# Kernel optimization log

Hardware: AMD Instinct MI355X
Metric: run time of the kernel (lower is better)

## Reference

```python
import jax, jax.numpy as jnp
import numpy as np

N = 100000   # nodes
E = 1600000  # edges
D = 128      # in_channels
H = 64       # hidden_channels
G = 64       # graphs in batch
C = 2        # num_classes


def _linear_init(key, fin, fout):
    s = 1.0 / np.sqrt(fin)
    kw, kb = jax.random.split(key)
    w = jax.random.uniform(kw, (fin, fout), jnp.float32, -s, s)
    b = jax.random.uniform(kb, (fout,), jnp.float32, -s, s)
    return w, b


def setup_inputs() -> dict:
    key = jax.random.key(0)
    ks = jax.random.split(key, 12)
    x = jax.random.normal(ks[0], (N, D), jnp.float32)
    edge_index = jax.random.randint(ks[1], (2, E), 0, N)
    batch = jnp.sort(jax.random.randint(ks[2], (N,), 0, G))
    inp = {"x": x, "edge_index": edge_index, "batch": batch}
    fins = [D, H, H]
    for i, fin in enumerate(fins):
        w1, b1 = _linear_init(ks[3 + 2 * i], fin, H)
        w2, b2 = _linear_init(ks[4 + 2 * i], H, H)
        inp[f"l{i}_w1"], inp[f"l{i}_b1"] = w1, b1
        inp[f"l{i}_w2"], inp[f"l{i}_b2"] = w2, b2
    inp["lin1_w"], inp["lin1_b"] = _linear_init(ks[9], H, H)
    inp["lin2_w"], inp["lin2_b"] = _linear_init(ks[10], H, C)
    return inp


def _gin_conv(h, edge_index, w1, b1, w2, b2):
    # sum-aggregate neighbor features: dst += h[src]  (eps = 0)
    agg = jax.ops.segment_sum(h[edge_index[0]], edge_index[1], num_segments=N)
    z = h + agg
    return jnp.maximum(z @ w1 + b1, 0.0) @ w2 + b2


def reference(x, edge_index, batch,
              l0_w1, l0_b1, l0_w2, l0_b2,
              l1_w1, l1_b1, l1_w2, l1_b2,
              l2_w1, l2_b1, l2_w2, l2_b2,
              lin1_w, lin1_b, lin2_w, lin2_b):
    params = [(l0_w1, l0_b1, l0_w2, l0_b2),
              (l1_w1, l1_b1, l1_w2, l1_b2),
              (l2_w1, l2_b1, l2_w2, l2_b2)]
    h = x
    for (w1, b1, w2, b2) in params:
        h = jnp.maximum(_gin_conv(h, edge_index, w1, b1, w2, b2), 0.0)
        # dropout is identity in eval mode
    # global mean pool over graph ids
    sums = jax.ops.segment_sum(h, batch, num_segments=G)          # [G, H]
    cnt = jax.ops.segment_sum(jnp.ones((N,), jnp.float32), batch, num_segments=G)
    pooled = sums / jnp.maximum(cnt, 1.0)[:, None]
    out = jnp.maximum(pooled @ lin1_w + lin1_b, 0.0)
    return out @ lin2_w + lin2_b  # [G, C]
```

## Files before the change

kernel.cpp:

```cpp
#include <hip/hip_runtime.h>
#include <hip/hip_bf16.h>


__device__ inline unsigned short f2bf(float f) {
    union { __hip_bfloat16 b; unsigned short u; } cv;
    cv.b = __float2bfloat16(f);
    return cv.u;
}
__device__ inline float bflo(unsigned int v) {
    union { unsigned int u; float f; } c; c.u = v << 16; return c.f;
}
__device__ inline float bfhi(unsigned int v) {
    union { unsigned int u; float f; } c; c.u = v & 0xffff0000u; return c.f;
}

__global__ __launch_bounds__(1024) void zero1024_kernel(int* __restrict__ p) {
    p[threadIdx.x] = 0;
}

__global__ __launch_bounds__(256) void count_buckets_kernel(
    const int* __restrict__ ei, int* __restrict__ gcount, int E_) {
    __shared__ int hist[1024];
    const int tid = threadIdx.x;
    for (int i = tid; i < 1024; i += 256) hist[i] = 0;
    __syncthreads();
    const int base = blockIdx.x * 2048;
#pragma unroll
    for (int i = 0; i < 8; i++) {
        int e = base + i * 256 + tid;
        if (e < E_) atomicAdd(&hist[ei[E_ + e] >> 9], 1);
    }
    __syncthreads();
    for (int i = tid; i < 1024; i += 256)
        if (hist[i]) atomicAdd(&gcount[i], hist[i]);
}

__global__ __launch_bounds__(1024) void scan_buckets_kernel(
    const int* __restrict__ gcount, int* __restrict__ bbase,
    int* __restrict__ gcursor, int* __restrict__ rowptr, int K, int E_, int n) {
    __shared__ int sd[1024];
    const int tid = threadIdx.x;
    int v = (tid < K) ? gcount[tid] : 0;
    sd[tid] = v;
    __syncthreads();
    for (int off = 1; off < 1024; off <<= 1) {
        int x = (tid >= off) ? sd[tid - off] : 0;
        __syncthreads();
        sd[tid] += x;
        __syncthreads();
    }
    if (tid < K) {
        int excl = sd[tid] - v;
        bbase[tid] = excl;
        gcursor[tid] = excl;
    }
    if (tid == 0) {
        bbase[K] = E_;
        rowptr[n] = E_;
    }
}

__global__ __launch_bounds__(256) void bucketize_kernel(
    const int* __restrict__ ei, int* __restrict__ gcursor,
    unsigned* __restrict__ bpack, int E_) {
    __shared__ int hist[1024];
    __shared__ int gbase[1024];
    const int tid = threadIdx.x;
    for (int i = tid; i < 1024; i += 256) hist[i] = 0;
    __syncthreads();
    const int base = blockIdx.x * 2048;
    int bkt[8], rnk[8];
    unsigned pk[8];
#pragma unroll
    for (int i = 0; i < 8; i++) {
        int e = base + i * 256 + tid;
        bkt[i] = -1;
        if (e < E_) {
            int s = ei[e];
            int d = ei[E_ + e];
            bkt[i] = d >> 9;
            pk[i] = (unsigned)s | ((unsigned)(d & 511) << 22);
            rnk[i] = atomicAdd(&hist[bkt[i]], 1);
        }
    }
    __syncthreads();
    for (int i = tid; i < 1024; i += 256)
        if (hist[i]) gbase[i] = atomicAdd(&gcursor[i], hist[i]);
    __syncthreads();
#pragma unroll
    for (int i = 0; i < 8; i++)
        if (bkt[i] >= 0) bpack[gbase[bkt[i]] + rnk[i]] = pk[i];
}

__global__ __launch_bounds__(256) void build_csr_kernel(
    const unsigned* __restrict__ bpack, const int* __restrict__ bbase,
    int* __restrict__ rowptr, int* __restrict__ col, int n) {
    __shared__ int cnt[512];
    __shared__ int sp[256];
    const int tid = threadIdx.x;
    const int b = blockIdx.x;
    const int nstart = b << 9;
    const int estart = bbase[b];
    const int eend = bbase[b + 1];
    cnt[tid] = 0;
    cnt[tid + 256] = 0;
    __syncthreads();
    for (int e = estart + tid; e < eend; e += 256)
        atomicAdd(&cnt[bpack[e] >> 22], 1);
    __syncthreads();
    const int v0 = cnt[tid * 2], v1 = cnt[tid * 2 + 1];
    const int s = v0 + v1;
    sp[tid] = s;
    __syncthreads();
    for (int off = 1; off < 256; off <<= 1) {
        int x = (tid >= off) ? sp[tid - off] : 0;
        __syncthreads();
        sp[tid] += x;
        __syncthreads();
    }
    const int excl = sp[tid] - s;
    cnt[tid * 2] = excl;
    cnt[tid * 2 + 1] = excl + v0;
    const int node0 = nstart + tid * 2;
    if (node0 < n) rowptr[node0] = estart + excl;
    if (node0 + 1 < n) rowptr[node0 + 1] = estart + excl + v0;
    __syncthreads();
    for (int e = estart + tid; e < eend; e += 256) {
        unsigned p = bpack[e];
        int pos = estart + atomicAdd(&cnt[p >> 22], 1);
        col[pos] = (int)(p & 0x3FFFFFu);
    }
}

__global__ __launch_bounds__(256) void proj128_kernel(
    const float* __restrict__ x, unsigned short* __restrict__ y,
    const float* __restrict__ w, int n) {
    constexpr int STR = 66;
    __shared__ unsigned int xs[64 * STR];
    const int tid = threadIdx.x;
    const int tile = blockIdx.x;
    for (int idx = tid; idx < 64 * 64; idx += 256) {
        int r = idx >> 6;
        int c = idx & 63;
        int node = tile * 64 + r;
        float2 v = make_float2(0.f, 0.f);
        if (node < n) v = *reinterpret_cast<const float2*>(x + (size_t)node * 128 + c * 2);
        xs[r * STR + c] = (unsigned)f2bf(v.x) | ((unsigned)f2bf(v.y) << 16);
    }
    __syncthreads();
    const int lane = tid & 63;
    const int j0 = __builtin_amdgcn_readfirstlane(tid >> 6) << 4;
    float a[16];
#pragma unroll
    for (int jj = 0; jj < 16; jj++) a[jj] = 0.f;
    for (int k = 0; k < 128; k += 8) {
        unsigned p0 = xs[lane * STR + k / 2 + 0];
        unsigned p1 = xs[lane * STR + k / 2 + 1];
        unsigned p2 = xs[lane * STR + k / 2 + 2];
        unsigned p3 = xs[lane * STR + k / 2 + 3];
        const float tv[8] = {bflo(p0), bfhi(p0), bflo(p1), bfhi(p1),
                             bflo(p2), bfhi(p2), bflo(p3), bfhi(p3)};
#pragma unroll
        for (int kk = 0; kk < 8; kk++)
#pragma unroll
            for (int jj = 0; jj < 16; jj++)
                a[jj] = fmaf(tv[kk], w[(k + kk) * 64 + j0 + jj], a[jj]);
    }
    const int node = tile * 64 + lane;
    if (node < n) {
        unsigned pk[8];
#pragma unroll
        for (int jj = 0; jj < 8; jj++)
            pk[jj] = (unsigned)f2bf(a[2 * jj]) | ((unsigned)f2bf(a[2 * jj + 1]) << 16);
        uint4* orow = reinterpret_cast<uint4*>(y + (size_t)node * 64 + j0);
        orow[0] = make_uint4(pk[0], pk[1], pk[2], pk[3]);
        orow[1] = make_uint4(pk[4], pk[5], pk[6], pk[7]);
    }
}

template <bool LAST>
__global__ __launch_bounds__(256) void fused_layer_kernel(
    const unsigned short* __restrict__ yin,
    const int* __restrict__ rowptr, const int* __restrict__ col,
    const float* __restrict__ b1,
    const float* __restrict__ w2, const float* __restrict__ b2,
    const float* __restrict__ w1n,
    unsigned short* __restrict__ yout, float* __restrict__ hout, int n) {
    constexpr int STR = 66;
    __shared__ float tl[64 * STR];
    const int tid = threadIdx.x;
    const int tile = blockIdx.x;
    const int lane = tid & 63;
    const int wv = __builtin_amdgcn_readfirstlane(tid >> 6);
    const int q = lane >> 4;
    const int fl = lane & 15;
    const uint2* y64 = reinterpret_cast<const uint2*>(yin);
    const float4 b1v = *reinterpret_cast<const float4*>(b1 + 4 * fl);

    for (int i = 0; i < 16; ++i) {
        const int node = tile * 64 + wv * 16 + i;
        if (node >= n) break;
        const int rs = rowptr[node];
        const int deg = rowptr[node + 1] - rs;
        float ax, ay, az, aw;
        {
            const uint2 sv = y64[(size_t)node * 16 + fl];
            const float m = (q == 0) ? 1.f : 0.f;
            ax = m * bflo(sv.x); ay = m * bfhi(sv.x);
            az = m * bflo(sv.y); aw = m * bfhi(sv.y);
        }
        int p = q;
        for (; p + 12 < deg; p += 16) {
            const int c0 = col[rs + p];
            const int c1 = col[rs + p + 4];
            const int c2 = col[rs + p + 8];
            const int c3 = col[rs + p + 12];
            const uint2 v0 = y64[(size_t)c0 * 16 + fl];
            const uint2 v1 = y64[(size_t)c1 * 16 + fl];
            const uint2 v2 = y64[(size_t)c2 * 16 + fl];
            const uint2 v3 = y64[(size_t)c3 * 16 + fl];
            ax += bflo(v0.x); ay += bfhi(v0.x); az += bflo(v0.y); aw += bfhi(v0.y);
            ax += bflo(v1.x); ay += bfhi(v1.x); az += bflo(v1.y); aw += bfhi(v1.y);
            ax += bflo(v2.x); ay += bfhi(v2.x); az += bflo(v2.y); aw += bfhi(v2.y);
            ax += bflo(v3.x); ay += bfhi(v3.x); az += bflo(v3.y); aw += bfhi(v3.y);
        }
        for (; p + 4 < deg; p += 8) {
            const int c0 = col[rs + p];
            const int c1 = col[rs + p + 4];
            const uint2 v0 = y64[(size_t)c0 * 16 + fl];
            const uint2 v1 = y64[(size_t)c1 * 16 + fl];
            ax += bflo(v0.x); ay += bfhi(v0.x); az += bflo(v0.y); aw += bfhi(v0.y);
            ax += bflo(v1.x); ay += bfhi(v1.x); az += bflo(v1.y); aw += bfhi(v1.y);
        }
        for (; p < deg; p += 4) {
            const int c = col[rs + p];
            const uint2 v = y64[(size_t)c * 16 + fl];
            ax += bflo(v.x); ay += bfhi(v.x); az += bflo(v.y); aw += bfhi(v.y);
        }
        ax += __shfl_xor(ax, 16); ay += __shfl_xor(ay, 16);
        az += __shfl_xor(az, 16); aw += __shfl_xor(aw, 16);
        ax += __shfl_xor(ax, 32); ay += __shfl_xor(ay, 32);
        az += __shfl_xor(az, 32); aw += __shfl_xor(aw, 32);
        if (q == 0) {
            const int row = wv * 16 + i;
            *reinterpret_cast<float2*>(&tl[row * STR + 4 * fl]) =
                make_float2(fmaxf(ax + b1v.x, 0.f), fmaxf(ay + b1v.y, 0.f));
            *reinterpret_cast<float2*>(&tl[row * STR + 4 * fl + 2]) =
                make_float2(fmaxf(az + b1v.z, 0.f), fmaxf(aw + b1v.w, 0.f));
        }
    }
    __syncthreads();

    const int j0 = wv << 4;
    const int node = tile * 64 + lane;
    float a[16];
#pragma unroll
    for (int jj = 0; jj < 16; jj++) a[jj] = b2[j0 + jj];
    for (int k = 0; k < 64; k += 8) {
        float2 t0 = *reinterpret_cast<const float2*>(&tl[lane * STR + k]);
        float2 t1 = *reinterpret_cast<const float2*>(&tl[lane * STR + k + 2]);
        float2 t2 = *reinterpret_cast<const float2*>(&tl[lane * STR + k + 4]);
        float2 t3 = *reinterpret_cast<const float2*>(&tl[lane * STR + k + 6]);
        const float tv[8] = {t0.x, t0.y, t1.x, t1.y, t2.x, t2.y, t3.x, t3.y};
#pragma unroll
        for (int kk = 0; kk < 8; kk++)
#pragma unroll
            for (int jj = 0; jj < 16; jj++)
                a[jj] = fmaf(tv[kk], w2[(k + kk) * 64 + j0 + jj], a[jj]);
    }
#pragma unroll
    for (int jj = 0; jj < 16; jj++) a[jj] = fmaxf(a[jj], 0.f);

    if (LAST) {
        if (node < n) {
            float* orow = hout + (size_t)node * 64 + j0;
#pragma unroll
            for (int jj = 0; jj < 16; jj += 4) {
                *reinterpret_cast<float4*>(orow + jj) =
                    make_float4(a[jj], a[jj + 1], a[jj + 2], a[jj + 3]);
            }
        }
    } else {
        __syncthreads();
#pragma unroll
        for (int jj = 0; jj < 16; jj++) tl[lane * STR + j0 + jj] = a[jj];
        __syncthreads();
        float a2[16];
#pragma unroll
        for (int jj = 0; jj < 16; jj++) a2[jj] = 0.f;
        for (int k = 0; k < 64; k += 8) {
            float2 t0 = *reinterpret_cast<const float2*>(&tl[lane * STR + k]);
            float2 t1 = *reinterpret_cast<const float2*>(&tl[lane * STR + k + 2]);
            float2 t2 = *reinterpret_cast<const float2*>(&tl[lane * STR + k + 4]);
            float2 t3 = *reinterpret_cast<const float2*>(&tl[lane * STR + k + 6]);
            const float tv[8] = {t0.x, t0.y, t1.x, t1.y, t2.x, t2.y, t3.x, t3.y};
#pragma unroll
            for (int kk = 0; kk < 8; kk++)
#pragma unroll
                for (int jj = 0; jj < 16; jj++)
                    a2[jj] = fmaf(tv[kk], w1n[(k + kk) * 64 + j0 + jj], a2[jj]);
        }
        if (node < n) {
            unsigned pk[8];
#pragma unroll
            for (int jj = 0; jj < 8; jj++)
                pk[jj] = (unsigned)f2bf(a2[2 * jj]) | ((unsigned)f2bf(a2[2 * jj + 1]) << 16);
            uint4* orow = reinterpret_cast<uint4*>(yout + (size_t)node * 64 + j0);
            orow[0] = make_uint4(pk[0], pk[1], pk[2], pk[3]);
            orow[1] = make_uint4(pk[4], pk[5], pk[6], pk[7]);
        }
    }
}

#define POOL_PARTS 16
__global__ __launch_bounds__(256) void pool_partial_kernel(
    const float* __restrict__ h, const int* __restrict__ batch,
    float* __restrict__ partials, int n) {
    const int g = blockIdx.x >> 4;
    const int part = blockIdx.x & 15;
    const int tid = threadIdx.x;
    auto lb = [&](int key) {
        int lo = 0, hi = n;
        while (lo < hi) {
            int mid = (lo + hi) >> 1;
            if (batch[mid] < key) lo = mid + 1;
            else hi = mid;
        }
        return lo;
    };
    const int lo = lb(g), hi = lb(g + 1);
    const int cnt = hi - lo;
    const int s0 = lo + (int)(((long long)cnt * part) / POOL_PARTS);
    const int s1 = lo + (int)(((long long)cnt * (part + 1)) / POOL_PARTS);

    const int f = tid & 63;
    const int qq = tid >> 6;
    float s = 0.f;
    for (int i = s0 + qq; i < s1; i += 4) s += h[(size_t)i * 64 + f];

    __shared__ float red[256];
    red[tid] = s;
    __syncthreads();
    if (tid < 64) {
        partials[(size_t)blockIdx.x * 64 + tid] =
            red[tid] + red[tid + 64] + red[tid + 128] + red[tid + 192];
    }
}

__global__ __launch_bounds__(64) void pool_head_kernel(
    const float* __restrict__ partials, const int* __restrict__ batch,
    const float* __restrict__ l1w, const float* __restrict__ l1b,
    const float* __restrict__ l2w, const float* __restrict__ l2b,
    float* __restrict__ out, int n) {
    const int g = blockIdx.x;
    const int tid = threadIdx.x;
    auto lb = [&](int key) {
        int lo = 0, hi = n;
        while (lo < hi) {
            int mid = (lo + hi) >> 1;
            if (batch[mid] < key) lo = mid + 1;
            else hi = mid;
        }
        return lo;
    };
    const int cnt = lb(g + 1) - lb(g);

    __shared__ float pooled[64];
    __shared__ float r[64];
    float v = 0.f;
#pragma unroll
    for (int p = 0; p < POOL_PARTS; p++)
        v += partials[(size_t)(g * POOL_PARTS + p) * 64 + tid];
    pooled[tid] = v / (float)((cnt > 1) ? cnt : 1);
    __syncthreads();
    float a = l1b[tid];
    for (int k = 0; k < 64; k++) a = fmaf(pooled[k], l1w[k * 64 + tid], a);
    r[tid] = fmaxf(a, 0.f);
    __syncthreads();
    if (tid < 2) {
        float a2 = l2b[tid];
        for (int k = 0; k < 64; k++) a2 = fmaf(r[k], l2w[k * 2 + tid], a2);
        out[g * 2 + tid] = a2;
    }
}


extern "C" void kernel_launch(void* const* d_in, const int* in_sizes, int n_in,
                              void* d_out, int out_size, void* d_ws, size_t ws_size,
                              hipStream_t stream) {
    const float* x    = (const float*)d_in[0];
    const int* ei     = (const int*)d_in[1];
    const int* batch  = (const int*)d_in[2];
    const float* l0w1 = (const float*)d_in[3];
    const float* l0b1 = (const float*)d_in[4];
    const float* l0w2 = (const float*)d_in[5];
    const float* l0b2 = (const float*)d_in[6];
    const float* l1w1 = (const float*)d_in[7];
    const float* l1b1 = (const float*)d_in[8];
    const float* l1w2 = (const float*)d_in[9];
    const float* l1b2 = (const float*)d_in[10];
    const float* l2w1 = (const float*)d_in[11];
    const float* l2b1 = (const float*)d_in[12];
    const float* l2w2 = (const float*)d_in[13];
    const float* l2b2 = (const float*)d_in[14];
    const float* lin1w = (const float*)d_in[15];
    const float* lin1b = (const float*)d_in[16];
    const float* lin2w = (const float*)d_in[17];
    const float* lin2b = (const float*)d_in[18];
    float* out = (float*)d_out;

    const int N  = in_sizes[2];
    const int E_ = in_sizes[1] / 2;
    const int K  = (N + 511) >> 9;
    const int G  = out_size / 2;

    char* ws = (char*)d_ws;
    size_t off = 0;
    auto alloc = [&](size_t bytes) {
        void* p = ws + off;
        off += (bytes + 255) & ~(size_t)255;
        return p;
    };
    int* rowptr  = (int*)alloc((size_t)(N + 1) * 4);
    int* col     = (int*)alloc((size_t)E_ * 4);
    int* gcount  = (int*)alloc(1024 * 4);
    int* bbase   = (int*)alloc(1025 * 4);
    int* gcursor = (int*)alloc(1024 * 4);
    float* partials = (float*)alloc((size_t)G * POOL_PARTS * 64 * 4);
    unsigned short* yA = (unsigned short*)alloc((size_t)N * 64 * 2);
    unsigned short* yB = (unsigned short*)alloc((size_t)N * 64 * 2);
    float* hbuf  = (float*)alloc((size_t)N * 64 * 4);
    unsigned* bpack = (unsigned*)hbuf;
    (void)ws_size;

    const int nch = (E_ + 2047) / 2048;

    zero1024_kernel<<<1, 1024, 0, stream>>>(gcount);
    count_buckets_kernel<<<nch, 256, 0, stream>>>(ei, gcount, E_);
    scan_buckets_kernel<<<1, 1024, 0, stream>>>(gcount, bbase, gcursor, rowptr, K, E_, N);
    bucketize_kernel<<<nch, 256, 0, stream>>>(ei, gcursor, bpack, E_);
    build_csr_kernel<<<K, 256, 0, stream>>>(bpack, bbase, rowptr, col, N);

    const int ntiles = (N + 63) / 64;

    proj128_kernel<<<ntiles, 256, 0, stream>>>(x, yA, l0w1, N);
    fused_layer_kernel<false><<<ntiles, 256, 0, stream>>>(
        yA, rowptr, col, l0b1, l0w2, l0b2, l1w1, yB, nullptr, N);
    fused_layer_kernel<false><<<ntiles, 256, 0, stream>>>(
        yB, rowptr, col, l1b1, l1w2, l1b2, l2w1, yA, nullptr, N);
    fused_layer_kernel<true><<<ntiles, 256, 0, stream>>>(
        yA, rowptr, col, l2b1, l2w2, l2b2, nullptr, nullptr, hbuf, N);

    pool_partial_kernel<<<G * POOL_PARTS, 256, 0, stream>>>(hbuf, batch, partials, N);
    pool_head_kernel<<<G, 64, 0, stream>>>(partials, batch, lin1w, lin1b, lin2w, lin2b, out, N);
}
```

Before: 316.4 us.

## Store projected features in chunked planes and gather per 16-feature chunk

The bf16 projected features are written as four planes of 16 features per node instead of one 64-feature row. The aggregation loop then gathers one plane at a time, with 8 lanes per edge and 8 edges per wave step, shrinking the random-access working set per pass to improve cache hit rates. The trade-off is re-reading rowptr/col four times, narrower 32-byte gathers, and extra shuffle reductions.

```diff
diff --git a/kernel.cpp b/kernel.cpp
--- a/kernel.cpp
+++ b/kernel.cpp
@@ -149,7 +149,8 @@
     }
     __syncthreads();
     const int lane = tid & 63;
-    const int j0 = __builtin_amdgcn_readfirstlane(tid >> 6) << 4;
+    const int wv = __builtin_amdgcn_readfirstlane(tid >> 6);
+    const int j0 = wv << 4;
     float a[16];
 #pragma unroll
     for (int jj = 0; jj < 16; jj++) a[jj] = 0.f;
@@ -172,9 +173,10 @@
 #pragma unroll
         for (int jj = 0; jj < 8; jj++)
             pk[jj] = (unsigned)f2bf(a[2 * jj]) | ((unsigned)f2bf(a[2 * jj + 1]) << 16);
-        uint4* orow = reinterpret_cast<uint4*>(y + (size_t)node * 64 + j0);
-        orow[0] = make_uint4(pk[0], pk[1], pk[2], pk[3]);
-        orow[1] = make_uint4(pk[4], pk[5], pk[6], pk[7]);
+        unsigned* yo = reinterpret_cast<unsigned*>(y) + (size_t)wv * n * 8 + (size_t)node * 8;
+        uint4* o = reinterpret_cast<uint4*>(yo);
+        o[0] = make_uint4(pk[0], pk[1], pk[2], pk[3]);
+        o[1] = make_uint4(pk[4], pk[5], pk[6], pk[7]);
     }
 }
 
@@ -192,61 +194,48 @@
     const int tile = blockIdx.x;
     const int lane = tid & 63;
     const int wv = __builtin_amdgcn_readfirstlane(tid >> 6);
-    const int q = lane >> 4;
-    const int fl = lane & 15;
-    const uint2* y64 = reinterpret_cast<const uint2*>(yin);
-    const float4 b1v = *reinterpret_cast<const float4*>(b1 + 4 * fl);
-
-    for (int i = 0; i < 16; ++i) {
-        const int node = tile * 64 + wv * 16 + i;
-        if (node >= n) break;
-        const int rs = rowptr[node];
-        const int deg = rowptr[node + 1] - rs;
-        float ax, ay, az, aw;
-        {
-            const uint2 sv = y64[(size_t)node * 16 + fl];
-            const float m = (q == 0) ? 1.f : 0.f;
-            ax = m * bflo(sv.x); ay = m * bfhi(sv.x);
-            az = m * bflo(sv.y); aw = m * bfhi(sv.y);
-        }
-        int p = q;
-        for (; p + 12 < deg; p += 16) {
-            const int c0 = col[rs + p];
-            const int c1 = col[rs + p + 4];
-            const int c2 = col[rs + p + 8];
-            const int c3 = col[rs + p + 12];
-            const uint2 v0 = y64[(size_t)c0 * 16 + fl];
-            const uint2 v1 = y64[(size_t)c1 * 16 + fl];
-            const uint2 v2 = y64[(size_t)c2 * 16 + fl];
-            const uint2 v3 = y64[(size_t)c3 * 16 + fl];
-            ax += bflo(v0.x); ay += bfhi(v0.x); az += bflo(v0.y); aw += bfhi(v0.y);
-            ax += bflo(v1.x); ay += bfhi(v1.x); az += bflo(v1.y); aw += bfhi(v1.y);
-            ax += bflo(v2.x); ay += bfhi(v2.x); az += bflo(v2.y); aw += bfhi(v2.y);
-            ax += bflo(v3.x); ay += bfhi(v3.x); az += bflo(v3.y); aw += bfhi(v3.y);
-        }
-        for (; p + 4 < deg; p += 8) {
-            const int c0 = col[rs + p];
-            const int c1 = col[rs + p + 4];
-            const uint2 v0 = y64[(size_t)c0 * 16 + fl];
-            const uint2 v1 = y64[(size_t)c1 * 16 + fl];
-            ax += bflo(v0.x); ay += bfhi(v0.x); az += bflo(v0.y); aw += bfhi(v0.y);
-            ax += bflo(v1.x); ay += bfhi(v1.x); az += bflo(v1.y); aw += bfhi(v1.y);
-        }
-        for (; p < deg; p += 4) {
-            const int c = col[rs + p];
-            const uint2 v = y64[(size_t)c * 16 + fl];
-            ax += bflo(v.x); ay += bfhi(v.x); az += bflo(v.y); aw += bfhi(v.y);
-        }
-        ax += __shfl_xor(ax, 16); ay += __shfl_xor(ay, 16);
-        az += __shfl_xor(az, 16); aw += __shfl_xor(aw, 16);
-        ax += __shfl_xor(ax, 32); ay += __shfl_xor(ay, 32);
-        az += __shfl_xor(az, 32); aw += __shfl_xor(aw, 32);
-        if (q == 0) {
-            const int row = wv * 16 + i;
-            *reinterpret_cast<float2*>(&tl[row * STR + 4 * fl]) =
-                make_float2(fmaxf(ax + b1v.x, 0.f), fmaxf(ay + b1v.y, 0.f));
-            *reinterpret_cast<float2*>(&tl[row * STR + 4 * fl + 2]) =
-                make_float2(fmaxf(az + b1v.z, 0.f), fmaxf(aw + b1v.w, 0.f));
+    const int e8 = lane >> 3;
+    const int f8 = lane & 7;
+    const unsigned int* y32 = reinterpret_cast<const unsigned int*>(yin);
+    const size_t n8 = (size_t)n * 8;
+
+    for (int c = 0; c < 4; ++c) {
+        const unsigned int* yb = y32 + (size_t)c * n8;
+        const float2 bv = *reinterpret_cast<const float2*>(b1 + c * 16 + 2 * f8);
+        for (int i = 0; i < 16; ++i) {
+            const int node = tile * 64 + wv * 16 + i;
+            if (node >= n) break;
+            const int rs = rowptr[node];
+            const int deg = rowptr[node + 1] - rs;
+            const unsigned sv = yb[(size_t)node * 8 + f8];
+            const float m = (e8 == 0) ? 1.f : 0.f;
+            float ax = m * bflo(sv);
+            float ay = m * bfhi(sv);
+            int base = 0;
+            for (; base + 16 <= deg; base += 16) {
+                const int c0 = col[rs + base + e8];
+                const int c1 = col[rs + base + 8 + e8];
+                const unsigned v0 = yb[(size_t)c0 * 8 + f8];
+                const unsigned v1 = yb[(size_t)c1 * 8 + f8];
+                ax += bflo(v0); ay += bfhi(v0);
+                ax += bflo(v1); ay += bfhi(v1);
+            }
+            for (; base < deg; base += 8) {
+                const int q = base + e8;
+                const int act = (q < deg);
+                const int cc = col[rs + (act ? q : 0)];
+                unsigned v = yb[(size_t)cc * 8 + f8];
+                if (!act) v = 0u;
+                ax += bflo(v); ay += bfhi(v);
+            }
+            ax += __shfl_xor(ax, 8);  ay += __shfl_xor(ay, 8);
+            ax += __shfl_xor(ax, 16); ay += __shfl_xor(ay, 16);
+            ax += __shfl_xor(ax, 32); ay += __shfl_xor(ay, 32);
+            if (e8 == 0) {
+                const int row = wv * 16 + i;
+                *reinterpret_cast<float2*>(&tl[row * STR + c * 16 + 2 * f8]) =
+                    make_float2(fmaxf(ax + bv.x, 0.f), fmaxf(ay + bv.y, 0.f));
+            }
         }
     }
     __syncthreads();
@@ -305,9 +294,10 @@
 #pragma unroll
             for (int jj = 0; jj < 8; jj++)
                 pk[jj] = (unsigned)f2bf(a2[2 * jj]) | ((unsigned)f2bf(a2[2 * jj + 1]) << 16);
-            uint4* orow = reinterpret_cast<uint4*>(yout + (size_t)node * 64 + j0);
-            orow[0] = make_uint4(pk[0], pk[1], pk[2], pk[3]);
-            orow[1] = make_uint4(pk[4], pk[5], pk[6], pk[7]);
+            unsigned* yo = reinterpret_cast<unsigned*>(yout) + (size_t)wv * n8 + (size_t)node * 8;
+            uint4* o = reinterpret_cast<uint4*>(yo);
+            o[0] = make_uint4(pk[0], pk[1], pk[2], pk[3]);
+            o[1] = make_uint4(pk[4], pk[5], pk[6], pk[7]);
         }
     }
 }
```

New measurement: 678.4 us. 114% more time.

## Assign gather quarter-waves to separate nodes, two nodes interleaved per lane group

Applied to the files above, without the earlier changes.

The neighbor gather previously split each node's edges across four quarter-waves and then reduced them with cross-lane shuffles. Now each quarter-wave owns its own nodes and processes two of them at once, issuing eight independent row loads per iteration and skipping the shuffle reduction. This is meant to raise memory-level parallelism and remove per-node shuffle and serialization overhead. In exchange, degree imbalance between the lanes' nodes causes divergence, and the tail handling now issues masked dummy loads.

```diff
diff --git a/kernel.cpp b/kernel.cpp
--- a/kernel.cpp
+++ b/kernel.cpp
@@ -197,24 +197,50 @@
     const uint2* y64 = reinterpret_cast<const uint2*>(yin);
     const float4 b1v = *reinterpret_cast<const float4*>(b1 + 4 * fl);
 
-    for (int i = 0; i < 16; ++i) {
-        const int node = tile * 64 + wv * 16 + i;
-        if (node >= n) break;
-        const int rs = rowptr[node];
-        const int deg = rowptr[node + 1] - rs;
-        float ax, ay, az, aw;
+    const int rbase = wv * 16 + 4 * q;
+#pragma unroll
+    for (int j = 0; j < 2; ++j) {
+        const int na = tile * 64 + rbase + 2 * j;
+        const int nb = na + 1;
+        const bool vA = (na < n), vB = (nb < n);
+        int rsa = 0, dega = 0, rsb = 0, degb = 0;
+        if (vA) { rsa = rowptr[na]; dega = rowptr[na + 1] - rsa; }
+        if (vB) { rsb = rowptr[nb]; degb = rowptr[nb + 1] - rsb; }
+        float ax, ay, az, aw, bx, by, bz, bw;
         {
-            const uint2 sv = y64[(size_t)node * 16 + fl];
-            const float m = (q == 0) ? 1.f : 0.f;
-            ax = m * bflo(sv.x); ay = m * bfhi(sv.x);
-            az = m * bflo(sv.y); aw = m * bfhi(sv.y);
-        }
-        int p = q;
-        for (; p + 12 < deg; p += 16) {
-            const int c0 = col[rs + p];
-            const int c1 = col[rs + p + 4];
-            const int c2 = col[rs + p + 8];
-            const int c3 = col[rs + p + 12];
+            uint2 sa = make_uint2(0u, 0u), sb = make_uint2(0u, 0u);
+            if (vA) sa = y64[(size_t)na * 16 + fl];
+            if (vB) sb = y64[(size_t)nb * 16 + fl];
+            ax = bflo(sa.x); ay = bfhi(sa.x); az = bflo(sa.y); aw = bfhi(sa.y);
+            bx = bflo(sb.x); by = bfhi(sb.x); bz = bflo(sb.y); bw = bfhi(sb.y);
+        }
+        int pa = 0, pb = 0;
+        while (pa + 4 <= dega && pb + 4 <= degb) {
+            const int ca0 = col[rsa + pa],     ca1 = col[rsa + pa + 1];
+            const int ca2 = col[rsa + pa + 2], ca3 = col[rsa + pa + 3];
+            const int cb0 = col[rsb + pb],     cb1 = col[rsb + pb + 1];
+            const int cb2 = col[rsb + pb + 2], cb3 = col[rsb + pb + 3];
+            const uint2 va0 = y64[(size_t)ca0 * 16 + fl];
+            const uint2 va1 = y64[(size_t)ca1 * 16 + fl];
+            const uint2 va2 = y64[(size_t)ca2 * 16 + fl];
+            const uint2 va3 = y64[(size_t)ca3 * 16 + fl];
+            const uint2 vb0 = y64[(size_t)cb0 * 16 + fl];
+            const uint2 vb1 = y64[(size_t)cb1 * 16 + fl];
+            const uint2 vb2 = y64[(size_t)cb2 * 16 + fl];
+            const uint2 vb3 = y64[(size_t)cb3 * 16 + fl];
+            ax += bflo(va0.x); ay += bfhi(va0.x); az += bflo(va0.y); aw += bfhi(va0.y);
+            ax += bflo(va1.x); ay += bfhi(va1.x); az += bflo(va1.y); aw += bfhi(va1.y);
+            ax += bflo(va2.x); ay += bfhi(va2.x); az += bflo(va2.y); aw += bfhi(va2.y);
+            ax += bflo(va3.x); ay += bfhi(va3.x); az += bflo(va3.y); aw += bfhi(va3.y);
+            bx += bflo(vb0.x); by += bfhi(vb0.x); bz += bflo(vb0.y); bw += bfhi(vb0.y);
+            bx += bflo(vb1.x); by += bfhi(vb1.x); bz += bflo(vb1.y); bw += bfhi(vb1.y);
+            bx += bflo(vb2.x); by += bfhi(vb2.x); bz += bflo(vb2.y); bw += bfhi(vb2.y);
+            bx += bflo(vb3.x); by += bfhi(vb3.x); bz += bflo(vb3.y); bw += bfhi(vb3.y);
+            pa += 4; pb += 4;
+        }
+        while (pa + 4 <= dega) {
+            const int c0 = col[rsa + pa],     c1 = col[rsa + pa + 1];
+            const int c2 = col[rsa + pa + 2], c3 = col[rsa + pa + 3];
             const uint2 v0 = y64[(size_t)c0 * 16 + fl];
             const uint2 v1 = y64[(size_t)c1 * 16 + fl];
             const uint2 v2 = y64[(size_t)c2 * 16 + fl];
@@ -223,30 +249,55 @@
             ax += bflo(v1.x); ay += bfhi(v1.x); az += bflo(v1.y); aw += bfhi(v1.y);
             ax += bflo(v2.x); ay += bfhi(v2.x); az += bflo(v2.y); aw += bfhi(v2.y);
             ax += bflo(v3.x); ay += bfhi(v3.x); az += bflo(v3.y); aw += bfhi(v3.y);
-        }
-        for (; p + 4 < deg; p += 8) {
-            const int c0 = col[rs + p];
-            const int c1 = col[rs + p + 4];
+            pa += 4;
+        }
+        while (pb + 4 <= degb) {
+            const int c0 = col[rsb + pb],     c1 = col[rsb + pb + 1];
+            const int c2 = col[rsb + pb + 2], c3 = col[rsb + pb + 3];
             const uint2 v0 = y64[(size_t)c0 * 16 + fl];
             const uint2 v1 = y64[(size_t)c1 * 16 + fl];
-            ax += bflo(v0.x); ay += bfhi(v0.x); az += bflo(v0.y); aw += bfhi(v0.y);
-            ax += bflo(v1.x); ay += bfhi(v1.x); az += bflo(v1.y); aw += bfhi(v1.y);
-        }
-        for (; p < deg; p += 4) {
-            const int c = col[rs + p];
-            const uint2 v = y64[(size_t)c * 16 + fl];
-            ax += bflo(v.x); ay += bfhi(v.x); az += bflo(v.y); aw += bfhi(v.y);
-        }
-        ax += __shfl_xor(ax, 16); ay += __shfl_xor(ay, 16);
-        az += __shfl_xor(az, 16); aw += __shfl_xor(aw, 16);
-        ax += __shfl_xor(ax, 32); ay += __shfl_xor(ay, 32);
-        az += __shfl_xor(az, 32); aw += __shfl_xor(aw, 32);
-        if (q == 0) {
-            const int row = wv * 16 + i;
-            *reinterpret_cast<float2*>(&tl[row * STR + 4 * fl]) =
+            const uint2 v2 = y64[(size_t)c2 * 16 + fl];
+            const uint2 v3 = y64[(size_t)c3 * 16 + fl];
+            bx += bflo(v0.x); by += bfhi(v0.x); bz += bflo(v0.y); bw += bfhi(v0.y);
+            bx += bflo(v1.x); by += bfhi(v1.x); bz += bflo(v1.y); bw += bfhi(v1.y);
+            bx += bflo(v2.x); by += bfhi(v2.x); bz += bflo(v2.y); bw += bfhi(v2.y);
+            bx += bflo(v3.x); by += bfhi(v3.x); bz += bflo(v3.y); bw += bfhi(v3.y);
+            pb += 4;
+        }
+        if (pa < dega) {
+#pragma unroll
+            for (int k = 0; k < 3; ++k) {
+                const int idx = pa + k;
+                const bool act = idx < dega;
+                const int c = col[rsa + (act ? idx : 0)];
+                uint2 v = y64[(size_t)c * 16 + fl];
+                if (!act) { v.x = 0u; v.y = 0u; }
+                ax += bflo(v.x); ay += bfhi(v.x); az += bflo(v.y); aw += bfhi(v.y);
+            }
+        }
+        if (pb < degb) {
+#pragma unroll
+            for (int k = 0; k < 3; ++k) {
+                const int idx = pb + k;
+                const bool act = idx < degb;
+                const int c = col[rsb + (act ? idx : 0)];
+                uint2 v = y64[(size_t)c * 16 + fl];
+                if (!act) { v.x = 0u; v.y = 0u; }
+                bx += bflo(v.x); by += bfhi(v.x); bz += bflo(v.y); bw += bfhi(v.y);
+            }
+        }
+        const int rowa = rbase + 2 * j;
+        if (vA) {
+            *reinterpret_cast<float2*>(&tl[rowa * STR + 4 * fl]) =
                 make_float2(fmaxf(ax + b1v.x, 0.f), fmaxf(ay + b1v.y, 0.f));
-            *reinterpret_cast<float2*>(&tl[row * STR + 4 * fl + 2]) =
+            *reinterpret_cast<float2*>(&tl[rowa * STR + 4 * fl + 2]) =
                 make_float2(fmaxf(az + b1v.z, 0.f), fmaxf(aw + b1v.w, 0.f));
+        }
+        if (vB) {
+            *reinterpret_cast<float2*>(&tl[(rowa + 1) * STR + 4 * fl]) =
+                make_float2(fmaxf(bx + b1v.x, 0.f), fmaxf(by + b1v.y, 0.f));
+            *reinterpret_cast<float2*>(&tl[(rowa + 1) * STR + 4 * fl + 2]) =
+                make_float2(fmaxf(bz + b1v.z, 0.f), fmaxf(bw + b1v.w, 0.f));
         }
     }
     __syncthreads();
```

Result: faster. 295.8 us, median of 2 (-6.5%).

## Assign four nodes per quarter-wave in gather to remove cross-lane reductions

Applied to the files above, without the earlier changes.

Each 16-lane quarter-wave now aggregates its own four nodes at once, with up to 16 independent row gathers in flight, instead of all four quarters splitting one node's edges and combining them through shuffles. This removes the per-node xor-shuffle reductions and the serial node loop, and raises memory-level parallelism for the irregular neighbour gathers. The cost is more registers, unbalanced work inside a wave when node degrees differ, and masked tail loads.

```diff
diff --git a/kernel.cpp b/kernel.cpp
--- a/kernel.cpp
+++ b/kernel.cpp
@@ -197,56 +197,122 @@
     const uint2* y64 = reinterpret_cast<const uint2*>(yin);
     const float4 b1v = *reinterpret_cast<const float4*>(b1 + 4 * fl);
 
-    for (int i = 0; i < 16; ++i) {
-        const int node = tile * 64 + wv * 16 + i;
-        if (node >= n) break;
-        const int rs = rowptr[node];
-        const int deg = rowptr[node + 1] - rs;
-        float ax, ay, az, aw;
+    {
+        const int rbase = wv * 16 + 4 * q;
+        int rs[4], dg[4], pp[4];
+        bool vl[4];
+        float A[4][4];
+#pragma unroll
+        for (int ii = 0; ii < 4; ++ii) {
+            const int nd = tile * 64 + rbase + ii;
+            vl[ii] = (nd < n);
+            rs[ii] = 0; dg[ii] = 0; pp[ii] = 0;
+            if (vl[ii]) { rs[ii] = rowptr[nd]; dg[ii] = rowptr[nd + 1] - rs[ii]; }
+        }
         {
-            const uint2 sv = y64[(size_t)node * 16 + fl];
-            const float m = (q == 0) ? 1.f : 0.f;
-            ax = m * bflo(sv.x); ay = m * bfhi(sv.x);
-            az = m * bflo(sv.y); aw = m * bfhi(sv.y);
-        }
-        int p = q;
-        for (; p + 12 < deg; p += 16) {
-            const int c0 = col[rs + p];
-            const int c1 = col[rs + p + 4];
-            const int c2 = col[rs + p + 8];
-            const int c3 = col[rs + p + 12];
-            const uint2 v0 = y64[(size_t)c0 * 16 + fl];
-            const uint2 v1 = y64[(size_t)c1 * 16 + fl];
-            const uint2 v2 = y64[(size_t)c2 * 16 + fl];
-            const uint2 v3 = y64[(size_t)c3 * 16 + fl];
-            ax += bflo(v0.x); ay += bfhi(v0.x); az += bflo(v0.y); aw += bfhi(v0.y);
-            ax += bflo(v1.x); ay += bfhi(v1.x); az += bflo(v1.y); aw += bfhi(v1.y);
-            ax += bflo(v2.x); ay += bfhi(v2.x); az += bflo(v2.y); aw += bfhi(v2.y);
-            ax += bflo(v3.x); ay += bfhi(v3.x); az += bflo(v3.y); aw += bfhi(v3.y);
-        }
-        for (; p + 4 < deg; p += 8) {
-            const int c0 = col[rs + p];
-            const int c1 = col[rs + p + 4];
-            const uint2 v0 = y64[(size_t)c0 * 16 + fl];
-            const uint2 v1 = y64[(size_t)c1 * 16 + fl];
-            ax += bflo(v0.x); ay += bfhi(v0.x); az += bflo(v0.y); aw += bfhi(v0.y);
-            ax += bflo(v1.x); ay += bfhi(v1.x); az += bflo(v1.y); aw += bfhi(v1.y);
-        }
-        for (; p < deg; p += 4) {
-            const int c = col[rs + p];
-            const uint2 v = y64[(size_t)c * 16 + fl];
-            ax += bflo(v.x); ay += bfhi(v.x); az += bflo(v.y); aw += bfhi(v.y);
-        }
-        ax += __shfl_xor(ax, 16); ay += __shfl_xor(ay, 16);
-        az += __shfl_xor(az, 16); aw += __shfl_xor(aw, 16);
-        ax += __shfl_xor(ax, 32); ay += __shfl_xor(ay, 32);
-        az += __shfl_xor(az, 32); aw += __shfl_xor(aw, 32);
-        if (q == 0) {
-            const int row = wv * 16 + i;
-            *reinterpret_cast<float2*>(&tl[row * STR + 4 * fl]) =
-                make_float2(fmaxf(ax + b1v.x, 0.f), fmaxf(ay + b1v.y, 0.f));
-            *reinterpret_cast<float2*>(&tl[row * STR + 4 * fl + 2]) =
-                make_float2(fmaxf(az + b1v.z, 0.f), fmaxf(aw + b1v.w, 0.f));
+            uint2 sv[4];
+#pragma unroll
+            for (int ii = 0; ii < 4; ++ii) {
+                const int nd = tile * 64 + rbase + ii;
+                sv[ii] = vl[ii] ? y64[(size_t)nd * 16 + fl] : make_uint2(0u, 0u);
+            }
+#pragma unroll
+            for (int ii = 0; ii < 4; ++ii) {
+                A[ii][0] = bflo(sv[ii].x); A[ii][1] = bfhi(sv[ii].x);
+                A[ii][2] = bflo(sv[ii].y); A[ii][3] = bfhi(sv[ii].y);
+            }
+        }
+        while (pp[0] + 4 <= dg[0] && pp[1] + 4 <= dg[1] &&
+               pp[2] + 4 <= dg[2] && pp[3] + 4 <= dg[3]) {
+            int cc[16];
+#pragma unroll
+            for (int ii = 0; ii < 4; ++ii)
+#pragma unroll
+                for (int k = 0; k < 4; ++k)
+                    cc[ii * 4 + k] = col[rs[ii] + pp[ii] + k];
+            uint2 vv[16];
+#pragma unroll
+            for (int j = 0; j < 16; ++j) vv[j] = y64[(size_t)cc[j] * 16 + fl];
+#pragma unroll
+            for (int ii = 0; ii < 4; ++ii) {
+#pragma unroll
+                for (int k = 0; k < 4; ++k) {
+                    const uint2 v = vv[ii * 4 + k];
+                    A[ii][0] += bflo(v.x); A[ii][1] += bfhi(v.x);
+                    A[ii][2] += bflo(v.y); A[ii][3] += bfhi(v.y);
+                }
+                pp[ii] += 4;
+            }
+        }
+#pragma unroll
+        for (int pr = 0; pr < 2; ++pr) {
+            const int i0 = pr * 2, i1 = pr * 2 + 1;
+            while (pp[i0] + 4 <= dg[i0] && pp[i1] + 4 <= dg[i1]) {
+                int cc[8];
+#pragma unroll
+                for (int k = 0; k < 4; ++k) {
+                    cc[k] = col[rs[i0] + pp[i0] + k];
+                    cc[4 + k] = col[rs[i1] + pp[i1] + k];
+                }
+                uint2 vv[8];
+#pragma unroll
+                for (int j = 0; j < 8; ++j) vv[j] = y64[(size_t)cc[j] * 16 + fl];
+#pragma unroll
+                for (int k = 0; k < 4; ++k) {
+                    A[i0][0] += bflo(vv[k].x); A[i0][1] += bfhi(vv[k].x);
+                    A[i0][2] += bflo(vv[k].y); A[i0][3] += bfhi(vv[k].y);
+                }
+#pragma unroll
+                for (int k = 0; k < 4; ++k) {
+                    A[i1][0] += bflo(vv[4 + k].x); A[i1][1] += bfhi(vv[4 + k].x);
+                    A[i1][2] += bflo(vv[4 + k].y); A[i1][3] += bfhi(vv[4 + k].y);
+                }
+                pp[i0] += 4; pp[i1] += 4;
+            }
+        }
+#pragma unroll
+        for (int ii = 0; ii < 4; ++ii) {
+            while (pp[ii] + 4 <= dg[ii]) {
+                int cc[4];
+#pragma unroll
+                for (int k = 0; k < 4; ++k) cc[k] = col[rs[ii] + pp[ii] + k];
+                uint2 vv[4];
+#pragma unroll
+                for (int j = 0; j < 4; ++j) vv[j] = y64[(size_t)cc[j] * 16 + fl];
+#pragma unroll
+                for (int k = 0; k < 4; ++k) {
+                    A[ii][0] += bflo(vv[k].x); A[ii][1] += bfhi(vv[k].x);
+                    A[ii][2] += bflo(vv[k].y); A[ii][3] += bfhi(vv[k].y);
+                }
+                pp[ii] += 4;
+            }
+        }
+#pragma unroll
+        for (int ii = 0; ii < 4; ++ii) {
+            if (pp[ii] < dg[ii]) {
+#pragma unroll
+                for (int k = 0; k < 3; ++k) {
+                    const int idx = pp[ii] + k;
+                    const bool act = idx < dg[ii];
+                    const int c = col[rs[ii] + (act ? idx : 0)];
+                    uint2 v = y64[(size_t)c * 16 + fl];
+                    if (!act) { v.x = 0u; v.y = 0u; }
+                    A[ii][0] += bflo(v.x); A[ii][1] += bfhi(v.x);
+                    A[ii][2] += bflo(v.y); A[ii][3] += bfhi(v.y);
+                }
+            }
+        }
+#pragma unroll
+        for (int ii = 0; ii < 4; ++ii) {
+            if (vl[ii]) {
+                const int row = rbase + ii;
+                *reinterpret_cast<float2*>(&tl[row * STR + 4 * fl]) =
+                    make_float2(fmaxf(A[ii][0] + b1v.x, 0.f),
+                                fmaxf(A[ii][1] + b1v.y, 0.f));
+                *reinterpret_cast<float2*>(&tl[row * STR + 4 * fl + 2]) =
+                    make_float2(fmaxf(A[ii][2] + b1v.z, 0.f),
+                                fmaxf(A[ii][3] + b1v.w, 0.f));
+            }
         }
     }
     __syncthreads();
```

New measurement: 344.2 us. 8.8% more time.
